# Performance work log

Hardware: AMD Instinct MI355X
Metric: run time of the kernel (lower is better)

The kernel has to match this reference:

```python
import jax, jax.numpy as jnp
import numpy as np

N = 100000      # nodes
E = 1600000     # edges (avg degree 16)
IN_FEATS = 128
HEADS = 4
OUT_FEATS = 16
NEG_SLOPE = 0.2
EPS = 1e-16


def setup_inputs() -> dict:
    key = jax.random.key(0)
    k1, k2, k3, k4, k5, k6 = jax.random.split(key, 6)
    feat = jax.random.normal(k1, (N, IN_FEATS), dtype=jnp.float32)
    # xavier-ish scale for params
    W = jax.random.normal(k2, (IN_FEATS, HEADS * OUT_FEATS), dtype=jnp.float32) * 0.1
    attn_l = jax.random.normal(k3, (1, HEADS, OUT_FEATS), dtype=jnp.float32) * 0.1
    attn_r = jax.random.normal(k4, (1, HEADS, OUT_FEATS), dtype=jnp.float32) * 0.1
    src_index = jax.random.randint(k5, (E,), 0, N, dtype=jnp.int32)
    trg_index = jax.random.randint(k6, (E,), 0, N, dtype=jnp.int32)
    return {"feat": feat, "W": W, "attn_l": attn_l, "attn_r": attn_r,
            "src_index": src_index, "trg_index": trg_index}


def reference(feat, W, attn_l, attn_r, src_index, trg_index):
    # dropout layers are identity in eval mode
    n = feat.shape[0]
    h = (feat @ W).reshape(n, HEADS, OUT_FEATS)            # [N,H,F]
    el = jnp.sum(h * attn_l, axis=-1)                      # [N,H]
    er = jnp.sum(h * attn_r, axis=-1)                      # [N,H]
    s = el[src_index] + er[trg_index]                      # [E,H] edge scores
    s = jnp.where(s > 0, s, NEG_SLOPE * s)                 # LeakyReLU(0.2)
    # neighborhood-aware softmax over incoming edges of each target node
    s = s - jnp.max(s)                                     # global max shift (as in source)
    e = jnp.exp(s)                                         # [E,H]
    denom = jax.ops.segment_sum(e, trg_index, num_segments=n)  # [N,H]
    attn = e / (denom[trg_index] + EPS)                    # [E,H]
    # weighted aggregation of lifted source features into target nodes
    msg = h[src_index] * attn[:, :, None]                  # [E,H,F]
    h_prime = jax.ops.segment_sum(msg, trg_index, num_segments=n)  # [N,H,F]
    return h_prime.reshape(n, HEADS * OUT_FEATS)
```

## Files before the change

### kernel.cpp

```cpp
#include <hip/hip_runtime.h>

typedef unsigned short ushort_t;
typedef __attribute__((ext_vector_type(8))) short bf16x8;
typedef __attribute__((ext_vector_type(4))) float f32x4v;

#define BN 128
#define LOGBN 7
#define CAP 3072
#define MAXBKT 1024

static __device__ __forceinline__ ushort_t f2bf(float f) {
  union { float f; unsigned int i; } v; v.f = f;
  unsigned int r = v.i + 0x7FFFu + ((v.i >> 16) & 1u);
  return (ushort_t)(r >> 16);
}
static __device__ __forceinline__ float leaky(float s) {
  return s > 0.f ? s : 0.2f * s;
}

__global__ __launch_bounds__(256) void packw_hist(
    const float* __restrict__ W, const float* __restrict__ attnl,
    const float* __restrict__ attnr, ushort_t* __restrict__ wfrag,
    const int* __restrict__ trg, int E, int nbkt,
    int* __restrict__ blockHist, int nb3, int epb)
{
  const int b = blockIdx.x;
  const int t = threadIdx.x;
  if (b == nb3) {
    __shared__ float sW[128 * 64];
    __shared__ float sAl[64], sAr[64];
    for (int i = t; i < 128 * 64 / 4; i += 256)
      ((float4*)sW)[i] = ((const float4*)W)[i];
    if (t < 64) sAl[t] = attnl[t];
    else if (t < 128) sAr[t - 64] = attnr[t - 64];
    __syncthreads();
    const int kc = t >> 6, l = t & 63;
    const int q = l >> 4, n = l & 15;
    #pragma unroll
    for (int tile = 0; tile < 5; ++tile) {
      #pragma unroll
      for (int j = 0; j < 8; ++j) {
        const int k = kc * 32 + q * 8 + j;
        float v = 0.f;
        if (tile < 4) {
          v = sW[k * 64 + tile * 16 + n];
        } else if (n < 4) {
          for (int f = 0; f < 16; ++f)
            v += sW[k * 64 + n * 16 + f] * sAl[n * 16 + f];
        } else if (n < 8) {
          const int hd = n - 4;
          for (int f = 0; f < 16; ++f)
            v += sW[k * 64 + hd * 16 + f] * sAr[hd * 16 + f];
        }
        wfrag[((tile * 4 + kc) * 64 + l) * 8 + j] = f2bf(v);
      }
    }
    return;
  }
  __shared__ int hist[MAXBKT];
  for (int i = t; i < nbkt; i += 256) hist[i] = 0;
  __syncthreads();
  const int start = b * epb;
  const int end = min(start + epb, E);
  for (int e = start + t; e < end; e += 256)
    atomicAdd(&hist[trg[e] >> LOGBN], 1);
  __syncthreads();
  for (int i = t; i < nbkt; i += 256) blockHist[b * nbkt + i] = hist[i];
}

__global__ __launch_bounds__(64) void bucket_scan(
    int* __restrict__ blockHist, int nb3, int nbkt, int* __restrict__ colTotal)
{
  const int b = blockIdx.x;
  const int l = threadIdx.x;
  int carry = 0;
  for (int r = 0; r * 64 < nb3; ++r) {
    const int i = r * 64 + l;
    int v = (i < nb3) ? blockHist[i * nbkt + b] : 0;
    int incl = v;
    #pragma unroll
    for (int d = 1; d < 64; d <<= 1) {
      int u = __shfl_up(incl, d, 64);
      if (l >= d) incl += u;
    }
    if (i < nb3) blockHist[i * nbkt + b] = carry + incl - v;
    carry += __shfl(incl, 63, 64);
  }
  if (l == 0) colTotal[b] = carry;
}

__global__ __launch_bounds__(64) void bucket_base(
    const int* __restrict__ colTotal, int nbkt, int* __restrict__ bucketBase)
{
  const int l = threadIdx.x;
  int carry = 0;
  for (int r = 0; r * 64 < nbkt; ++r) {
    const int i = r * 64 + l;
    int v = (i < nbkt) ? colTotal[i] : 0;
    int incl = v;
    #pragma unroll
    for (int d = 1; d < 64; d <<= 1) {
      int u = __shfl_up(incl, d, 64);
      if (l >= d) incl += u;
    }
    if (i < nbkt) bucketBase[i] = carry + incl - v;
    carry += __shfl(incl, 63, 64);
  }
  if (l == 0) bucketBase[nbkt] = carry;
}

__global__ __launch_bounds__(256) void bucket_scatter(
    const int* __restrict__ src, const int* __restrict__ trg, int E, int nbkt,
    const int* __restrict__ blockHist, const int* __restrict__ bucketBase,
    unsigned int* __restrict__ binned, int epb)
{
  __shared__ int cursor[MAXBKT];
  const int t = threadIdx.x, b = blockIdx.x;
  for (int i = t; i < nbkt; i += 256)
    cursor[i] = bucketBase[i] + blockHist[b * nbkt + i];
  __syncthreads();
  const int start = b * epb;
  const int end = min(start + epb, E);
  for (int e = start + t; e < end; e += 256) {
    const int ti = trg[e];
    const int bkt = ti >> LOGBN;
    const int pos = atomicAdd(&cursor[bkt], 1);
    binned[pos] = ((unsigned int)src[e] << LOGBN) | (unsigned int)(ti & (BN - 1));
  }
}

__global__ __launch_bounds__(256) void fine_sort(
    unsigned int* __restrict__ binned, const int* __restrict__ bucketBase,
    int* __restrict__ rowbeg, int* __restrict__ rowend, int N)
{
  __shared__ unsigned int pld[CAP];
  __shared__ int hist[BN];
  __shared__ int cursor[BN];
  __shared__ int wtot[2];
  const int t = threadIdx.x;
  const int b = blockIdx.x;
  const int base = bucketBase[b];
  const int cn = min(bucketBase[b + 1] - base, CAP);
  unsigned int* slot = binned + base;

  if (t < BN) hist[t] = 0;
  __syncthreads();
  for (int i = t; i < cn; i += 256) {
    const unsigned int pv = slot[i];
    pld[i] = pv;
    atomicAdd(&hist[pv & (BN - 1)], 1);
  }
  __syncthreads();

  int v = 0, incl = 0;
  if (t < BN) {
    v = hist[t];
    incl = v;
    #pragma unroll
    for (int d = 1; d < 64; d <<= 1) {
      int u = __shfl_up(incl, d, 64);
      if ((t & 63) >= d) incl += u;
    }
  }
  if (t < BN && (t & 63) == 63) wtot[t >> 6] = incl;
  __syncthreads();
  if (t < BN) {
    const int excl = incl - v + ((t >= 64) ? wtot[0] : 0);
    cursor[t] = excl;
    const int node = b * BN + t;
    if (node < N) {
      rowbeg[node] = base + excl;
      rowend[node] = base + excl + v;
    }
  }
  __syncthreads();

  for (int i = t; i < cn; i += 256) {
    const unsigned int pv = pld[i];
    const int pos = atomicAdd(&cursor[pv & (BN - 1)], 1);
    slot[pos] = pv >> LOGBN;
  }
}

__global__ __launch_bounds__(256) void gat_linear(
    const float* __restrict__ feat, const ushort_t* __restrict__ wfrag,
    ushort_t* __restrict__ h_out, float* __restrict__ el, float* __restrict__ er,
    float* __restrict__ blockmax2, int N)
{
  __shared__ ushort_t sFb[64 * 136];
  __shared__ float wmax[8];
  const int t = threadIdx.x;
  const int b = blockIdx.x;
  const int w = t >> 6, l = t & 63;
  const int q = l >> 4, m = l & 15;

  const float4* gF = (const float4*)(feat + (size_t)b * 64 * 128);
  #pragma unroll
  for (int i = 0; i < 8; ++i) {
    const int idx = i * 256 + t;
    const int node = idx >> 5, off = idx & 31;
    float4 v = make_float4(0.f, 0.f, 0.f, 0.f);
    if (b * 64 + node < N) v = gF[idx];
    unsigned int p0 = ((unsigned int)f2bf(v.y) << 16) | f2bf(v.x);
    unsigned int p1 = ((unsigned int)f2bf(v.w) << 16) | f2bf(v.z);
    *(uint2*)(sFb + node * 136 + off * 4) = make_uint2(p0, p1);
  }
  __syncthreads();

  bf16x8 a[4];
  const ushort_t* arow = sFb + (w * 16 + m) * 136 + q * 8;
  #pragma unroll
  for (int kc = 0; kc < 4; ++kc)
    a[kc] = *(const bf16x8*)(arow + kc * 32);

  #pragma unroll
  for (int tile = 0; tile < 4; ++tile) {
    f32x4v acc = {0.f, 0.f, 0.f, 0.f};
    #pragma unroll
    for (int kc = 0; kc < 4; ++kc) {
      bf16x8 bfr = *(const bf16x8*)(wfrag + ((tile * 4 + kc) * 64 + l) * 8);
      acc = __builtin_amdgcn_mfma_f32_16x16x32_bf16(a[kc], bfr, acc, 0, 0, 0);
    }
    #pragma unroll
    for (int r = 0; r < 4; ++r) {
      const int gn = b * 64 + w * 16 + q * 4 + r;
      if (gn < N) h_out[(size_t)gn * 64 + tile * 16 + m] = f2bf(acc[r]);
    }
  }

  f32x4v acc4 = {0.f, 0.f, 0.f, 0.f};
  #pragma unroll
  for (int kc = 0; kc < 4; ++kc) {
    bf16x8 bfr = *(const bf16x8*)(wfrag + ((4 * 4 + kc) * 64 + l) * 8);
    acc4 = __builtin_amdgcn_mfma_f32_16x16x32_bf16(a[kc], bfr, acc4, 0, 0, 0);
  }
  float mel = -1e30f, mer = -1e30f;
  #pragma unroll
  for (int r = 0; r < 4; ++r) {
    const int gn = b * 64 + w * 16 + q * 4 + r;
    const float v = acc4[r];
    if (m < 4) {
      if (gn < N) el[gn * 4 + m] = v;
      mel = fmaxf(mel, v);
    } else if (m < 8) {
      if (gn < N) er[gn * 4 + (m - 4)] = v;
      mer = fmaxf(mer, v);
    }
  }
  #pragma unroll
  for (int o = 1; o <= 32; o <<= 1) {
    mel = fmaxf(mel, __shfl_xor(mel, o, 64));
    mer = fmaxf(mer, __shfl_xor(mer, o, 64));
  }
  if (l == 0) { wmax[w * 2] = mel; wmax[w * 2 + 1] = mer; }
  __syncthreads();
  if (t == 0) {
    float aa = fmaxf(fmaxf(wmax[0], wmax[2]), fmaxf(wmax[4], wmax[6]));
    float cc = fmaxf(fmaxf(wmax[1], wmax[3]), fmaxf(wmax[5], wmax[7]));
    blockmax2[b * 2] = aa;
    blockmax2[b * 2 + 1] = cc;
  }
}

__global__ __launch_bounds__(256) void gmax_reduce(
    const float* __restrict__ blockmax2, int nbL, float* __restrict__ gmaxM)
{
  __shared__ float wmg[8];
  const int t = threadIdx.x, l = t & 63, w = t >> 6;
  float mel = -1e30f, mer = -1e30f;
  for (int i = t; i < nbL; i += 256) {
    mel = fmaxf(mel, blockmax2[i * 2]);
    mer = fmaxf(mer, blockmax2[i * 2 + 1]);
  }
  #pragma unroll
  for (int o = 1; o <= 32; o <<= 1) {
    mel = fmaxf(mel, __shfl_xor(mel, o, 64));
    mer = fmaxf(mer, __shfl_xor(mer, o, 64));
  }
  if (l == 0) { wmg[w * 2] = mel; wmg[w * 2 + 1] = mer; }
  __syncthreads();
  if (t == 0) {
    float aa = fmaxf(fmaxf(wmg[0], wmg[2]), fmaxf(wmg[4], wmg[6]));
    float cc = fmaxf(fmaxf(wmg[1], wmg[3]), fmaxf(wmg[5], wmg[7]));
    gmaxM[0] = fmaxf(0.f, aa + cc);
  }
}

#define UNPACK_FMA(hv, p, acc) do { \
  union { unsigned int i; float f; } c_; \
  c_.i = (hv).x << 16;          acc[0] += c_.f * (p); \
  c_.i = (hv).x & 0xffff0000u;  acc[1] += c_.f * (p); \
  c_.i = (hv).y << 16;          acc[2] += c_.f * (p); \
  c_.i = (hv).y & 0xffff0000u;  acc[3] += c_.f * (p); \
  c_.i = (hv).z << 16;          acc[4] += c_.f * (p); \
  c_.i = (hv).z & 0xffff0000u;  acc[5] += c_.f * (p); \
  c_.i = (hv).w << 16;          acc[6] += c_.f * (p); \
  c_.i = (hv).w & 0xffff0000u;  acc[7] += c_.f * (p); \
} while (0)

__global__ __launch_bounds__(256) void gat_agg(
    const unsigned int* __restrict__ csrsrc, const int* __restrict__ rowbeg,
    const int* __restrict__ rowend,
    const float4* __restrict__ el4, const float4* __restrict__ er4,
    const ushort_t* __restrict__ hbf, const float* __restrict__ gmaxM,
    float* __restrict__ out, int N)
{
  __shared__ float sP[4 * 64 * 4];
  __shared__ int sS[4 * 64];
  const int t = threadIdx.x;
  const int l = t & 63;
  const int w = t >> 6;
  const int nbase = blockIdx.x * 16 + w * 4;
  const int rg = l >> 3;
  const int cg = l & 7;
  const int hd2 = cg >> 1;
  const int ks = l >> 4;
  const int le = l & 15;
  const float M = gmaxM[0];
  float* sPw = sP + w * 256;
  int* sSw = sS + w * 64;
  const ushort_t* hcg = hbf + cg * 8;

  const int nk = nbase + ks;
  int rs = 0, re = 0;
  if (nk < N) { rs = rowbeg[nk]; re = rowend[nk]; }
  const float4 ernk = (rs < re) ? er4[nk]
                                : make_float4(0.f, 0.f, 0.f, 0.f);
  int deg = re - rs;
  deg = max(deg, __shfl_xor(deg, 16, 64));
  deg = max(deg, __shfl_xor(deg, 32, 64));
  const int chunks = (deg + 15) >> 4;

  float aA[8] = {0.f,0.f,0.f,0.f,0.f,0.f,0.f,0.f};
  float aB[8] = {0.f,0.f,0.f,0.f,0.f,0.f,0.f,0.f};
  float dA = 0.f, dB = 0.f;

  for (int c = 0; c < chunks; ++c) {
    int sn = 0;
    float4 pv = make_float4(0.f, 0.f, 0.f, 0.f);
    const int ei = rs + c * 16 + le;
    if (ei < re) {
      sn = (int)csrsrc[ei];
      const float4 a = el4[sn];
      pv.x = __expf(leaky(a.x + ernk.x) - M);
      pv.y = __expf(leaky(a.y + ernk.y) - M);
      pv.z = __expf(leaky(a.z + ernk.z) - M);
      pv.w = __expf(leaky(a.w + ernk.w) - M);
    }
    *(float4*)(sPw + l * 4) = pv;
    sSw[l] = sn;

    const int rem = min(deg - c * 16, 16);
    const int jmax = (rem + 3) >> 2;
    for (int j = 0; j < jmax; ++j) {
      const int iA = ((rg >> 2) * 16) + (rg & 3) + j * 4;
      const int iB = iA + 32;
      const int sA = sSw[iA];
      const int sB = sSw[iB];
      const float pA = sPw[iA * 4 + hd2];
      const float pB = sPw[iB * 4 + hd2];
      const uint4 hA = *(const uint4*)(hcg + (size_t)sA * 64);
      const uint4 hB = *(const uint4*)(hcg + (size_t)sB * 64);
      UNPACK_FMA(hA, pA, aA);
      UNPACK_FMA(hB, pB, aB);
      dA += pA;
      dB += pB;
    }
  }

  #pragma unroll
  for (int o = 8; o <= 16; o <<= 1) {
    #pragma unroll
    for (int i = 0; i < 8; ++i) {
      aA[i] += __shfl_xor(aA[i], o, 64);
      aB[i] += __shfl_xor(aB[i], o, 64);
    }
    dA += __shfl_xor(dA, o, 64);
    dB += __shfl_xor(dB, o, 64);
  }
  if ((rg & 3) == 0) {
    const int nA = nbase + (rg >> 2);
    const int nB = nA + 2;
    const float rA = 1.0f / (dA + 1e-16f);
    const float rB = 1.0f / (dB + 1e-16f);
    if (nA < N) {
      float4* orow = (float4*)(out + (size_t)nA * 64 + cg * 8);
      orow[0] = make_float4(aA[0] * rA, aA[1] * rA, aA[2] * rA, aA[3] * rA);
      orow[1] = make_float4(aA[4] * rA, aA[5] * rA, aA[6] * rA, aA[7] * rA);
    }
    if (nB < N) {
      float4* orow = (float4*)(out + (size_t)nB * 64 + cg * 8);
      orow[0] = make_float4(aB[0] * rB, aB[1] * rB, aB[2] * rB, aB[3] * rB);
      orow[1] = make_float4(aB[4] * rB, aB[5] * rB, aB[6] * rB, aB[7] * rB);
    }
  }
}

extern "C" void kernel_launch(void* const* d_in, const int* in_sizes, int n_in,
                              void* d_out, int out_size, void* d_ws, size_t ws_size,
                              hipStream_t stream) {
  const float* feat  = (const float*)d_in[0];
  const float* W     = (const float*)d_in[1];
  const float* attnl = (const float*)d_in[2];
  const float* attnr = (const float*)d_in[3];
  const int* src = (const int*)d_in[4];
  const int* trg = (const int*)d_in[5];
  float* out = (float*)d_out;

  const int N = in_sizes[0] / 128;
  const int E = in_sizes[4];

  const int nbL  = (N + 63) / 64;
  const int nbkt = (N + BN - 1) >> LOGBN;
  const int nb3  = 256;
  const int epb  = (E + nb3 - 1) / nb3;

  char* p = (char*)d_ws;
  auto take = [&](size_t bytes) -> char* {
    char* r = p;
    p += (bytes + 255) & ~(size_t)255;
    return r;
  };
  ushort_t* h_bf  = (ushort_t*)take((size_t)N * 64 * 2);
  float* el       = (float*)take((size_t)N * 16);
  float* er       = (float*)take((size_t)N * 16);
  unsigned int* binned = (unsigned int*)take((size_t)E * 4);
  int* rowbeg     = (int*)take((size_t)N * 4);
  int* rowend     = (int*)take((size_t)N * 4);
  ushort_t* wfrag = (ushort_t*)take(5 * 4 * 64 * 8 * 2);
  int* blockHist  = (int*)take((size_t)nb3 * nbkt * 4);
  int* colTotal   = (int*)take((size_t)nbkt * 4);
  int* bucketBase = (int*)take((size_t)(nbkt + 1) * 4);
  float* blockmax2 = (float*)take((size_t)nbL * 2 * 4);
  float* gmaxM    = (float*)take(256);

  packw_hist<<<nb3 + 1, 256, 0, stream>>>(W, attnl, attnr, wfrag,
                                          trg, E, nbkt, blockHist, nb3, epb);
  bucket_scan<<<nbkt, 64, 0, stream>>>(blockHist, nb3, nbkt, colTotal);
  bucket_base<<<1, 64, 0, stream>>>(colTotal, nbkt, bucketBase);
  bucket_scatter<<<nb3, 256, 0, stream>>>(src, trg, E, nbkt, blockHist,
                                          bucketBase, binned, epb);
  fine_sort<<<nbkt, 256, 0, stream>>>(binned, bucketBase, rowbeg, rowend, N);
  gat_linear<<<nbL, 256, 0, stream>>>(feat, wfrag, h_bf, el, er,
                                      blockmax2, N);
  gmax_reduce<<<1, 256, 0, stream>>>(blockmax2, nbL, gmaxM);
  gat_agg<<<(N + 15) / 16, 256, 0, stream>>>(binned, rowbeg, rowend,
                                             (const float4*)el,
                                             (const float4*)er, h_bf,
                                             gmaxM, out, N);
}
```

Before: 207.7 us.

## Fold global-max reduce into fine_sort and batch gather loads in aggregation

Merges the single-block gmax_reduce kernel into block 0 of fine_sort and moves gat_linear earlier so its block maxima are ready, which removes one kernel launch from the chain. In gat_agg, the variable inner loop over edge groups is replaced by up to four independent gathers issued before any FMA, so more memory loads are in flight per wave. The cost is higher register pressure in gat_agg, which may lower occupancy.

```diff
diff --git a/kernel.cpp b/kernel.cpp
--- a/kernel.cpp
+++ b/kernel.cpp
@@ -129,59 +129,6 @@
   }
 }
 
-__global__ __launch_bounds__(256) void fine_sort(
-    unsigned int* __restrict__ binned, const int* __restrict__ bucketBase,
-    int* __restrict__ rowbeg, int* __restrict__ rowend, int N)
-{
-  __shared__ unsigned int pld[CAP];
-  __shared__ int hist[BN];
-  __shared__ int cursor[BN];
-  __shared__ int wtot[2];
-  const int t = threadIdx.x;
-  const int b = blockIdx.x;
-  const int base = bucketBase[b];
-  const int cn = min(bucketBase[b + 1] - base, CAP);
-  unsigned int* slot = binned + base;
-
-  if (t < BN) hist[t] = 0;
-  __syncthreads();
-  for (int i = t; i < cn; i += 256) {
-    const unsigned int pv = slot[i];
-    pld[i] = pv;
-    atomicAdd(&hist[pv & (BN - 1)], 1);
-  }
-  __syncthreads();
-
-  int v = 0, incl = 0;
-  if (t < BN) {
-    v = hist[t];
-    incl = v;
-    #pragma unroll
-    for (int d = 1; d < 64; d <<= 1) {
-      int u = __shfl_up(incl, d, 64);
-      if ((t & 63) >= d) incl += u;
-    }
-  }
-  if (t < BN && (t & 63) == 63) wtot[t >> 6] = incl;
-  __syncthreads();
-  if (t < BN) {
-    const int excl = incl - v + ((t >= 64) ? wtot[0] : 0);
-    cursor[t] = excl;
-    const int node = b * BN + t;
-    if (node < N) {
-      rowbeg[node] = base + excl;
-      rowend[node] = base + excl + v;
-    }
-  }
-  __syncthreads();
-
-  for (int i = t; i < cn; i += 256) {
-    const unsigned int pv = pld[i];
-    const int pos = atomicAdd(&cursor[pv & (BN - 1)], 1);
-    slot[pos] = pv >> LOGBN;
-  }
-}
-
 __global__ __launch_bounds__(256) void gat_linear(
     const float* __restrict__ feat, const ushort_t* __restrict__ wfrag,
     ushort_t* __restrict__ h_out, float* __restrict__ el, float* __restrict__ er,
@@ -262,27 +209,77 @@
   }
 }
 
-__global__ __launch_bounds__(256) void gmax_reduce(
+__global__ __launch_bounds__(256) void fine_sort(
+    unsigned int* __restrict__ binned, const int* __restrict__ bucketBase,
+    int* __restrict__ rowbeg, int* __restrict__ rowend, int N,
     const float* __restrict__ blockmax2, int nbL, float* __restrict__ gmaxM)
 {
+  __shared__ unsigned int pld[CAP];
+  __shared__ int hist[BN];
+  __shared__ int cursor[BN];
+  __shared__ int wtot[2];
   __shared__ float wmg[8];
-  const int t = threadIdx.x, l = t & 63, w = t >> 6;
-  float mel = -1e30f, mer = -1e30f;
-  for (int i = t; i < nbL; i += 256) {
-    mel = fmaxf(mel, blockmax2[i * 2]);
-    mer = fmaxf(mer, blockmax2[i * 2 + 1]);
-  }
-  #pragma unroll
-  for (int o = 1; o <= 32; o <<= 1) {
-    mel = fmaxf(mel, __shfl_xor(mel, o, 64));
-    mer = fmaxf(mer, __shfl_xor(mer, o, 64));
-  }
-  if (l == 0) { wmg[w * 2] = mel; wmg[w * 2 + 1] = mer; }
-  __syncthreads();
-  if (t == 0) {
+  const int t = threadIdx.x;
+  const int b = blockIdx.x;
+  const int base = bucketBase[b];
+  const int cn = min(bucketBase[b + 1] - base, CAP);
+  unsigned int* slot = binned + base;
+
+  if (t < BN) hist[t] = 0;
+  if (b == 0) {
+    const int l = t & 63, w = t >> 6;
+    float mel = -1e30f, mer = -1e30f;
+    for (int i = t; i < nbL; i += 256) {
+      mel = fmaxf(mel, blockmax2[i * 2]);
+      mer = fmaxf(mer, blockmax2[i * 2 + 1]);
+    }
+    #pragma unroll
+    for (int o = 1; o <= 32; o <<= 1) {
+      mel = fmaxf(mel, __shfl_xor(mel, o, 64));
+      mer = fmaxf(mer, __shfl_xor(mer, o, 64));
+    }
+    if (l == 0) { wmg[w * 2] = mel; wmg[w * 2 + 1] = mer; }
+  }
+  __syncthreads();
+  if (b == 0 && t == 0) {
     float aa = fmaxf(fmaxf(wmg[0], wmg[2]), fmaxf(wmg[4], wmg[6]));
     float cc = fmaxf(fmaxf(wmg[1], wmg[3]), fmaxf(wmg[5], wmg[7]));
     gmaxM[0] = fmaxf(0.f, aa + cc);
+  }
+  for (int i = t; i < cn; i += 256) {
+    const unsigned int pv = slot[i];
+    pld[i] = pv;
+    atomicAdd(&hist[pv & (BN - 1)], 1);
+  }
+  __syncthreads();
+
+  int v = 0, incl = 0;
+  if (t < BN) {
+    v = hist[t];
+    incl = v;
+    #pragma unroll
+    for (int d = 1; d < 64; d <<= 1) {
+      int u = __shfl_up(incl, d, 64);
+      if ((t & 63) >= d) incl += u;
+    }
+  }
+  if (t < BN && (t & 63) == 63) wtot[t >> 6] = incl;
+  __syncthreads();
+  if (t < BN) {
+    const int excl = incl - v + ((t >= 64) ? wtot[0] : 0);
+    cursor[t] = excl;
+    const int node = b * BN + t;
+    if (node < N) {
+      rowbeg[node] = base + excl;
+      rowend[node] = base + excl + v;
+    }
+  }
+  __syncthreads();
+
+  for (int i = t; i < cn; i += 256) {
+    const unsigned int pv = pld[i];
+    const int pos = atomicAdd(&cursor[pv & (BN - 1)], 1);
+    slot[pos] = pv >> LOGBN;
   }
 }
 
@@ -296,6 +293,16 @@
   c_.i = (hv).z & 0xffff0000u;  acc[5] += c_.f * (p); \
   c_.i = (hv).w << 16;          acc[6] += c_.f * (p); \
   c_.i = (hv).w & 0xffff0000u;  acc[7] += c_.f * (p); \
+} while (0)
+
+#define LOADJ(j, hA_, hB_, qA_, qB_) do { \
+  const int i_ = iA0 + (j) * 4; \
+  const int sA_ = sSw[i_]; \
+  const int sB_ = sSw[i_ + 32]; \
+  qA_ = sPw[i_ * 4 + hd2]; \
+  qB_ = sPw[(i_ + 32) * 4 + hd2]; \
+  hA_ = *(const uint4*)(hcg + (size_t)sA_ * 64); \
+  hB_ = *(const uint4*)(hcg + (size_t)sB_ * 64); \
 } while (0)
 
 __global__ __launch_bounds__(256) void gat_agg(
@@ -320,6 +327,7 @@
   float* sPw = sP + w * 256;
   int* sSw = sS + w * 64;
   const ushort_t* hcg = hbf + cg * 8;
+  const int iA0 = ((rg >> 2) * 16) + (rg & 3);
 
   const int nk = nbase + ks;
   int rs = 0, re = 0;
@@ -352,19 +360,26 @@
 
     const int rem = min(deg - c * 16, 16);
     const int jmax = (rem + 3) >> 2;
-    for (int j = 0; j < jmax; ++j) {
-      const int iA = ((rg >> 2) * 16) + (rg & 3) + j * 4;
-      const int iB = iA + 32;
-      const int sA = sSw[iA];
-      const int sB = sSw[iB];
-      const float pA = sPw[iA * 4 + hd2];
-      const float pB = sPw[iB * 4 + hd2];
-      const uint4 hA = *(const uint4*)(hcg + (size_t)sA * 64);
-      const uint4 hB = *(const uint4*)(hcg + (size_t)sB * 64);
-      UNPACK_FMA(hA, pA, aA);
-      UNPACK_FMA(hB, pB, aB);
-      dA += pA;
-      dB += pB;
+    uint4 h0A, h0B, h1A, h1B, h2A, h2B, h3A, h3B;
+    float q0A, q0B, q1A, q1B, q2A, q2B, q3A, q3B;
+    LOADJ(0, h0A, h0B, q0A, q0B);
+    if (jmax > 1) LOADJ(1, h1A, h1B, q1A, q1B);
+    if (jmax > 2) LOADJ(2, h2A, h2B, q2A, q2B);
+    if (jmax > 3) LOADJ(3, h3A, h3B, q3A, q3B);
+
+    UNPACK_FMA(h0A, q0A, aA); UNPACK_FMA(h0B, q0B, aB);
+    dA += q0A; dB += q0B;
+    if (jmax > 1) {
+      UNPACK_FMA(h1A, q1A, aA); UNPACK_FMA(h1B, q1B, aB);
+      dA += q1A; dB += q1B;
+    }
+    if (jmax > 2) {
+      UNPACK_FMA(h2A, q2A, aA); UNPACK_FMA(h2B, q2B, aB);
+      dA += q2A; dB += q2B;
+    }
+    if (jmax > 3) {
+      UNPACK_FMA(h3A, q3A, aA); UNPACK_FMA(h3B, q3B, aB);
+      dA += q3A; dB += q3B;
     }
   }
 
@@ -436,14 +451,14 @@
 
   packw_hist<<<nb3 + 1, 256, 0, stream>>>(W, attnl, attnr, wfrag,
                                           trg, E, nbkt, blockHist, nb3, epb);
+  gat_linear<<<nbL, 256, 0, stream>>>(feat, wfrag, h_bf, el, er,
+                                      blockmax2, N);
   bucket_scan<<<nbkt, 64, 0, stream>>>(blockHist, nb3, nbkt, colTotal);
   bucket_base<<<1, 64, 0, stream>>>(colTotal, nbkt, bucketBase);
   bucket_scatter<<<nb3, 256, 0, stream>>>(src, trg, E, nbkt, blockHist,
                                           bucketBase, binned, epb);
-  fine_sort<<<nbkt, 256, 0, stream>>>(binned, bucketBase, rowbeg, rowend, N);
-  gat_linear<<<nbL, 256, 0, stream>>>(feat, wfrag, h_bf, el, er,
-                                      blockmax2, N);
-  gmax_reduce<<<1, 256, 0, stream>>>(blockmax2, nbL, gmaxM);
+  fine_sort<<<nbkt, 256, 0, stream>>>(binned, bucketBase, rowbeg, rowend, N,
+                                      blockmax2, nbL, gmaxM);
   gat_agg<<<(N + 15) / 16, 256, 0, stream>>>(binned, rowbeg, rowend,
                                              (const float4*)el,
                                              (const float4*)er, h_bf,
```

Result: slower. 220.7 us (+6.3%).
